# Performance work log

Hardware: AMD Instinct MI355X
Metric: run time of the kernel (lower is better)

The kernel has to match this reference:

```python
import jax, jax.numpy as jnp
import numpy as np

NQ = 18          # num_qubits
DEPTH = 3        # circuit_depth
DIM = 2 ** NQ    # state-vector length
STATE_DIM = 256
HIDDEN = 64
ACTION_DIM = 18
BATCH = 4096


def _apply_1q(sv, g, q):
    # apply 2x2 gate g to qubit q (qubit 0 = most-significant index bit, matching the kron order)
    pre, post = 2 ** q, 2 ** (NQ - q - 1)
    s = sv.reshape(pre, 2, post)
    return jnp.einsum('ab,ibj->iaj', g, s).reshape(-1)


def _apply_cnot(sv, at):
    # CNOT with target at reshape-axis `at`, control at axis `at+1` (adjacent, control less significant)
    pre, post = 2 ** at, 2 ** (NQ - at - 2)
    s = sv.reshape(pre, 2, 2, post)           # (pre, target, control, post)
    out = jnp.stack([s[:, :, 0, :], s[:, ::-1, 1, :]], axis=2)
    return out.reshape(-1)


def _circuit(theta, xc):
    sv = jnp.zeros(DIM, jnp.complex64).at[0].set(1.0)
    th = theta.reshape(DEPTH, NQ, 3)
    for layer in range(DEPTH):
        for q in range(NQ):
            a, b, c = th[layer, q, 0], th[layer, q, 1], th[layer, q, 2]
            ca = jnp.cos(a / 2).astype(jnp.complex64)
            sa = jnp.sin(a / 2).astype(jnp.complex64)
            rx = jnp.stack([jnp.stack([ca, -1j * sa]), jnp.stack([-1j * sa, ca])])
            cb = jnp.cos(b / 2).astype(jnp.complex64)
            sb = jnp.sin(b / 2).astype(jnp.complex64)
            ry = jnp.stack([jnp.stack([cb, -sb]), jnp.stack([sb, cb])])
            ez = jnp.exp(-0.5j * c.astype(jnp.complex64))
            z0 = jnp.zeros_like(ez)
            rz = jnp.stack([jnp.stack([ez, z0]), jnp.stack([z0, jnp.conj(ez)])])
            sv = _apply_1q(sv, rx, q)
            sv = _apply_1q(sv, ry, q)
            sv = _apply_1q(sv, rz, q)
        # original CNOT uses little-endian bit positions: control=q -> axis NQ-1-q, target=q+1 -> axis NQ-2-q
        for q in range(NQ - 1):
            sv = _apply_cnot(sv, NQ - 2 - q)
    # _encode_classical_input: flatten, normalize, add into state prefix, renormalize
    x = xc.reshape(-1)
    xn = jnp.linalg.norm(x)
    x = jnp.where(xn > 0, x / xn.astype(jnp.complex64), x)
    m = min(DIM, x.shape[0])
    sv = sv.at[:m].add(x[:m])
    return sv / jnp.linalg.norm(sv).astype(jnp.complex64)


def setup_inputs() -> dict:
    key = jax.random.key(0)
    ks = jax.random.split(key, 16)
    r = lambda k, shp, s: jax.random.normal(k, shp, jnp.float32) * s
    return {
        'state': r(ks[0], (BATCH, STATE_DIM), 1.0),
        'enc_w1': r(ks[1], (STATE_DIM, HIDDEN), 0.06),
        'enc_b1': jnp.zeros((HIDDEN,), jnp.float32),
        'enc_w2': r(ks[2], (HIDDEN, 2 * NQ), 0.12),
        'enc_b2': jnp.zeros((2 * NQ,), jnp.float32),
        'qparams': r(ks[3], (DEPTH * NQ * 3,), 0.1),
        'dec_w1': r(ks[4], (2 * DIM, HIDDEN), 0.0015),
        'dec_b1': jnp.zeros((HIDDEN,), jnp.float32),
        'dec_w2': r(ks[5], (HIDDEN, ACTION_DIM), 0.12),
        'dec_b2': jnp.zeros((ACTION_DIM,), jnp.float32),
        'val_w1': r(ks[6], (2 * DIM, HIDDEN), 0.0015),
        'val_b1': jnp.zeros((HIDDEN,), jnp.float32),
        'val_w2': r(ks[7], (HIDDEN, 1), 0.12),
        'val_b2': jnp.zeros((1,), jnp.float32),
    }


def reference(state, enc_w1, enc_b1, enc_w2, enc_b2, qparams,
              dec_w1, dec_b1, dec_w2, dec_b2,
              val_w1, val_b1, val_w2, val_b2):
    h = jax.nn.relu(state @ enc_w1 + enc_b1)
    enc = h @ enc_w2 + enc_b2                     # [B, 2*NQ]
    amp, ph = enc[:, :NQ], enc[:, NQ:]
    xc = amp.astype(jnp.complex64) * jnp.exp(1j * ph.astype(jnp.complex64))  # torch.polar
    sv = _circuit(qparams, xc)                    # [2^NQ] complex64
    cl = jnp.concatenate([sv.real, sv.imag])      # [2^(NQ+1)] float32
    logits = jax.nn.relu(cl @ dec_w1 + dec_b1) @ dec_w2 + dec_b2
    value = jax.nn.relu(cl @ val_w1 + val_b1) @ val_w2 + val_b2
    return logits, value
```

## Files before the change

kernel.cpp:

```cpp
#include <hip/hip_runtime.h>
#include <cstdint>
#include <cstddef>


#define NQb   18
#define DIMSZ 262144
#define PMASK 0x3FFFF
#define XLEN  73728

typedef float2 cplx;
typedef float f4 __attribute__((ext_vector_type(4)));

__device__ __forceinline__ cplx cmul(cplx a, cplx b) {
  return make_float2(a.x*b.x - a.y*b.y, a.x*b.y + a.y*b.x);
}
__device__ __forceinline__ cplx cadd(cplx a, cplx b) {
  return make_float2(a.x + b.x, a.y + b.y);
}

__global__ void k_prep(const float* __restrict__ qp, cplx* __restrict__ Ug,
                       cplx* __restrict__ prodLow, cplx* __restrict__ prodHigh,
                       float* __restrict__ accs) {
  __shared__ cplx Ush[54][4];
  int t = threadIdx.x;
  for (int k = t; k < 4352; k += 256) accs[k] = 0.0f;
  if (t < 54) {
    float a = qp[t*3+0], b = qp[t*3+1], c = qp[t*3+2];
    float ca = cosf(0.5f*a), sa = sinf(0.5f*a);
    float cb = cosf(0.5f*b), sb = sinf(0.5f*b);
    float cc = cosf(0.5f*c), sc = sinf(0.5f*c);
    cplx m00 = make_float2( cb*ca,  sb*sa);
    cplx m01 = make_float2(-sb*ca, -cb*sa);
    cplx m10 = make_float2( sb*ca, -cb*sa);
    cplx m11 = make_float2( cb*ca, -sb*sa);
    cplx e0 = make_float2(cc, -sc), e1 = make_float2(cc, sc);
    cplx u00 = cmul(e0, m00), u01 = cmul(e0, m01);
    cplx u10 = cmul(e1, m10), u11 = cmul(e1, m11);
    Ush[t][0] = u00; Ush[t][1] = u01; Ush[t][2] = u10; Ush[t][3] = u11;
    Ug[t*4+0] = u00; Ug[t*4+1] = u01; Ug[t*4+2] = u10; Ug[t*4+3] = u11;
  }
  __syncthreads();
  for (int m = t; m < 4096; m += blockDim.x) {
    cplx v = make_float2(1.f, 0.f);
    for (int p = 0; p < 12; ++p) {
      int q = 17 - p;
      cplx f = ((m >> p) & 1) ? Ush[q][2] : Ush[q][0];
      v = cmul(v, f);
    }
    prodLow[m] = v;
  }
  if (t < 64) {
    cplx v = make_float2(1.f, 0.f);
    for (int p = 12; p < 18; ++p) {
      int q = 17 - p;
      cplx f = ((t >> (p - 12)) & 1) ? Ush[q][2] : Ush[q][0];
      v = cmul(v, f);
    }
    prodHigh[t] = v;
  }
}

__global__ __launch_bounds__(256) void k_enc(
    const float* __restrict__ state, const float* __restrict__ w1,
    const float* __restrict__ b1, const float* __restrict__ w2,
    const float* __restrict__ b2, float* __restrict__ xRe,
    float* __restrict__ xIm, float* __restrict__ xn2) {
  __shared__ float sState[4][256];
  __shared__ float hS[4][64];
  __shared__ float encS[4][36];
  __shared__ float wsum[4];
  int t = threadIdx.x;
  int r = t >> 6, j = t & 63;
  const float4* st4 =
      reinterpret_cast<const float4*>(state + (size_t)blockIdx.x * 1024);
  reinterpret_cast<float4*>(&sState[0][0])[t] = st4[t];
  __syncthreads();
  float a0 = 0.f, a1 = 0.f, a2 = 0.f, a3 = 0.f;
#pragma unroll 4
  for (int k = 0; k < 256; k += 4) {
    a0 = fmaf(sState[r][k+0], w1[(k+0)*64 + j], a0);
    a1 = fmaf(sState[r][k+1], w1[(k+1)*64 + j], a1);
    a2 = fmaf(sState[r][k+2], w1[(k+2)*64 + j], a2);
    a3 = fmaf(sState[r][k+3], w1[(k+3)*64 + j], a3);
  }
  hS[r][j] = fmaxf((a0 + a1) + (a2 + a3) + b1[j], 0.f);
  __syncthreads();
  if (j < 36) {
    float a = b2[j];
#pragma unroll 8
    for (int k = 0; k < 64; ++k) a = fmaf(hS[r][k], w2[k*36 + j], a);
    encS[r][j] = a;
  }
  __syncthreads();
  float lsum = 0.f;
  if (j < 18) {
    float amp = encS[r][j], ph = encS[r][18 + j];
    float sp, cp;
    sincosf(ph, &sp, &cp);
    int row = blockIdx.x*4 + r;
    xRe[row*18 + j] = amp * cp;
    xIm[row*18 + j] = amp * sp;
    lsum = amp * amp;
  }
  for (int off = 32; off > 0; off >>= 1) lsum += __shfl_down(lsum, off, 64);
  if (j == 0) wsum[r] = lsum;
  __syncthreads();
  if (t == 0) atomicAdd(xn2, wsum[0] + wsum[1] + wsum[2] + wsum[3]);
}

__global__ __launch_bounds__(512) void k_gatesLow(
    const cplx* __restrict__ Ug, const cplx* __restrict__ prodLow,
    const cplx* __restrict__ prodHigh, const cplx* __restrict__ svIn,
    cplx* __restrict__ svOut, int layer, int mode) {
  __shared__ float sRe[1024], sIm[1024];
  int t = threadIdx.x;
  int base = blockIdx.x << 10;
  for (int e = t; e < 1024; e += 512) {
    int i = base + e;
    int src = (i ^ (i << 1)) & PMASK;
    cplx v;
    if (mode == 0) v = cmul(prodHigh[src >> 12], prodLow[src & 4095]);
    else           v = svIn[src];
    sRe[e] = v.x; sIm[e] = v.y;
  }
  __syncthreads();
  for (int p = 0; p < 10; ++p) {
    int q = 17 - p;
    const cplx* U = Ug + (layer*18 + q)*4;
    cplx u00 = U[0], u01 = U[1], u10 = U[2], u11 = U[3];
    {
      int k = t;
      int i0 = ((k >> p) << (p + 1)) | (k & ((1 << p) - 1));
      int i1 = i0 | (1 << p);
      cplx a = make_float2(sRe[i0], sIm[i0]);
      cplx b = make_float2(sRe[i1], sIm[i1]);
      cplx na = cadd(cmul(u00, a), cmul(u01, b));
      cplx nb = cadd(cmul(u10, a), cmul(u11, b));
      sRe[i0] = na.x; sIm[i0] = na.y;
      sRe[i1] = nb.x; sIm[i1] = nb.y;
    }
    __syncthreads();
  }
  for (int e = t; e < 1024; e += 512)
    svOut[base + e] = make_float2(sRe[e], sIm[e]);
}

__global__ __launch_bounds__(512) void k_gatesHigh(
    const cplx* __restrict__ Ug, cplx* __restrict__ sv, int layer) {
  __shared__ float tRe[1024], tIm[1024];
  int t = threadIdx.x;
  int l0 = blockIdx.x << 2;
  for (int e = t; e < 1024; e += 512) {
    int h = e >> 2, j = e & 3;
    cplx v = sv[h*1024 + l0 + j];
    tRe[e] = v.x; tIm[e] = v.y;
  }
  __syncthreads();
  for (int ph = 0; ph < 8; ++ph) {
    int q = 7 - ph;
    const cplx* U = Ug + (layer*18 + q)*4;
    cplx u00 = U[0], u01 = U[1], u10 = U[2], u11 = U[3];
    {
      int kh = t >> 2, j = t & 3;
      int h0 = ((kh >> ph) << (ph + 1)) | (kh & ((1 << ph) - 1));
      int h1 = h0 | (1 << ph);
      int i0 = h0*4 + j, i1 = h1*4 + j;
      cplx a = make_float2(tRe[i0], tIm[i0]);
      cplx b = make_float2(tRe[i1], tIm[i1]);
      cplx na = cadd(cmul(u00, a), cmul(u01, b));
      cplx nb = cadd(cmul(u10, a), cmul(u11, b));
      tRe[i0] = na.x; tIm[i0] = na.y;
      tRe[i1] = nb.x; tIm[i1] = nb.y;
    }
    __syncthreads();
  }
  for (int e = t; e < 1024; e += 512) {
    int h = e >> 2, j = e & 3;
    sv[h*1024 + l0 + j] = make_float2(tRe[e], tIm[e]);
  }
}

__global__ __launch_bounds__(256) void k_combine(
    const cplx* __restrict__ svIn, const float* __restrict__ xRe,
    const float* __restrict__ xIm, const float* __restrict__ xn2,
    float* __restrict__ cl, float* __restrict__ L2acc) {
  int t = threadIdx.x;
  float xs = xn2[0];
  float invXn = (xs > 0.f) ? (1.0f / sqrtf(xs)) : 1.0f;
  float lsum = 0.f;
  for (int u = 0; u < 4; ++u) {
    int i = blockIdx.x*1024 + u*256 + t;
    int src = (i ^ (i << 1)) & PMASK;
    cplx v = svIn[src];
    if (i < XLEN) {
      v.x = fmaf(xRe[i], invXn, v.x);
      v.y = fmaf(xIm[i], invXn, v.y);
    }
    cl[i] = v.x;
    cl[DIMSZ + i] = v.y;
    lsum += v.x*v.x + v.y*v.y;
  }
  for (int off = 32; off > 0; off >>= 1) lsum += __shfl_down(lsum, off, 64);
  if ((t & 63) == 0) atomicAdd(L2acc, lsum);
}

#define GLOAD(dst, ptr) \
  asm volatile("global_load_dwordx4 %0, %1, off nt" : "=v"(dst) : "v"(ptr))

#define VMWAIT(N, x0,x1,x2,x3,x4,x5,x6,x7) do {                      \
    asm volatile("s_waitcnt vmcnt(" #N ")"                           \
        : "+v"(x0), "+v"(x1), "+v"(x2), "+v"(x3),                    \
          "+v"(x4), "+v"(x5), "+v"(x6), "+v"(x7));                   \
    __builtin_amdgcn_sched_barrier(0);                               \
  } while (0)

#define CONSUME(g, w0,w1,w2,w3,w4,w5,w6,w7) do {                     \
    const int rr = (g)*128 + ro;                                     \
    float s0 = clS[rr+  0], s1 = clS[rr+ 16];                        \
    float s2 = clS[rr+ 32], s3 = clS[rr+ 48];                        \
    float s4 = clS[rr+ 64], s5 = clS[rr+ 80];                        \
    float s6 = clS[rr+ 96], s7 = clS[rr+112];                        \
    ax = fmaf(s0, w0[0], ax); ay = fmaf(s0, w0[1], ay);              \
    az = fmaf(s0, w0[2], az); aw = fmaf(s0, w0[3], aw);              \
    ax = fmaf(s1, w1[0], ax); ay = fmaf(s1, w1[1], ay);              \
    az = fmaf(s1, w1[2], az); aw = fmaf(s1, w1[3], aw);              \
    ax = fmaf(s2, w2[0], ax); ay = fmaf(s2, w2[1], ay);              \
    az = fmaf(s2, w2[2], az); aw = fmaf(s2, w2[3], aw);              \
    ax = fmaf(s3, w3[0], ax); ay = fmaf(s3, w3[1], ay);              \
    az = fmaf(s3, w3[2], az); aw = fmaf(s3, w3[3], aw);              \
    ax = fmaf(s4, w4[0], ax); ay = fmaf(s4, w4[1], ay);              \
    az = fmaf(s4, w4[2], az); aw = fmaf(s4, w4[3], aw);              \
    ax = fmaf(s5, w5[0], ax); ay = fmaf(s5, w5[1], ay);              \
    az = fmaf(s5, w5[2], az); aw = fmaf(s5, w5[3], aw);              \
    ax = fmaf(s6, w6[0], ax); ay = fmaf(s6, w6[1], ay);              \
    az = fmaf(s6, w6[2], az); aw = fmaf(s6, w6[3], aw);              \
    ax = fmaf(s7, w7[0], ax); ay = fmaf(s7, w7[1], ay);              \
    az = fmaf(s7, w7[2], az); aw = fmaf(s7, w7[3], aw);              \
  } while (0)

__global__ __launch_bounds__(256) void k_matvec(
    const float* __restrict__ cl, const float* __restrict__ Wdec,
    const float* __restrict__ Wval, float* __restrict__ dots_rep) {
  __shared__ float clS[512];
  __shared__ float red[1024];
  int t = threadIdx.x;
  int mat = blockIdx.x & 1;
  int chunk = blockIdx.x >> 1;
  size_t r0 = (size_t)chunk * 512;
  if (t < 128)
    reinterpret_cast<float4*>(clS)[t] =
        reinterpret_cast<const float4*>(cl + r0)[t];
  __syncthreads();
  const float* Wb = (mat ? Wval : Wdec) + r0*64 + (size_t)((t & 15)*4);
  const int ro = t >> 4;
  const float* p0 = Wb + (size_t)ro * 64;
  const float* p1 = p0 + 1024;
  const float* p2 = p0 + 2048;
  const float* p3 = p0 + 3072;
  const float* p4 = p0 + 4096;
  const float* p5 = p0 + 5120;
  const float* p6 = p0 + 6144;
  const float* p7 = p0 + 7168;
  float ax = 0.f, ay = 0.f, az = 0.f, aw = 0.f;
  f4 A0, A1, A2, A3, A4, A5, A6, A7;
  f4 B0, B1, B2, B3, B4, B5, B6, B7;
  GLOAD(A0, p0);        GLOAD(A1, p1);        GLOAD(A2, p2);
  GLOAD(A3, p3);        GLOAD(A4, p4);        GLOAD(A5, p5);
  GLOAD(A6, p6);        GLOAD(A7, p7);
  GLOAD(B0, p0 + 8192); GLOAD(B1, p1 + 8192); GLOAD(B2, p2 + 8192);
  GLOAD(B3, p3 + 8192); GLOAD(B4, p4 + 8192); GLOAD(B5, p5 + 8192);
  GLOAD(B6, p6 + 8192); GLOAD(B7, p7 + 8192);
  VMWAIT(8, A0, A1, A2, A3, A4, A5, A6, A7);
  CONSUME(0, A0, A1, A2, A3, A4, A5, A6, A7);
  GLOAD(A0, p0 + 16384); GLOAD(A1, p1 + 16384); GLOAD(A2, p2 + 16384);
  GLOAD(A3, p3 + 16384); GLOAD(A4, p4 + 16384); GLOAD(A5, p5 + 16384);
  GLOAD(A6, p6 + 16384); GLOAD(A7, p7 + 16384);
  VMWAIT(8, B0, B1, B2, B3, B4, B5, B6, B7);
  CONSUME(1, B0, B1, B2, B3, B4, B5, B6, B7);
  GLOAD(B0, p0 + 24576); GLOAD(B1, p1 + 24576); GLOAD(B2, p2 + 24576);
  GLOAD(B3, p3 + 24576); GLOAD(B4, p4 + 24576); GLOAD(B5, p5 + 24576);
  GLOAD(B6, p6 + 24576); GLOAD(B7, p7 + 24576);
  VMWAIT(8, A0, A1, A2, A3, A4, A5, A6, A7);
  CONSUME(2, A0, A1, A2, A3, A4, A5, A6, A7);
  VMWAIT(0, B0, B1, B2, B3, B4, B5, B6, B7);
  CONSUME(3, B0, B1, B2, B3, B4, B5, B6, B7);

  red[t*4+0] = ax; red[t*4+1] = ay; red[t*4+2] = az; red[t*4+3] = aw;
  __syncthreads();
  if (t < 64) {
    int ci0 = t >> 2, jj = t & 3;
    float sum = 0.f;
#pragma unroll
    for (int r2 = 0; r2 < 16; ++r2) sum += red[(r2*16 + ci0)*4 + jj];
    int slot = chunk & 31;
    atomicAdd(&dots_rep[slot*128 + mat*64 + t], sum);
  }
}

__global__ void k_final(const float* __restrict__ dots_rep,
                        const float* __restrict__ L2acc,
                        const float* __restrict__ db1,
                        const float* __restrict__ dw2,
                        const float* __restrict__ db2,
                        const float* __restrict__ vb1,
                        const float* __restrict__ vw2,
                        const float* __restrict__ vb2,
                        float* __restrict__ out) {
  __shared__ float hd[64], hv[64];
  int t = threadIdx.x;
  float sd = 0.f, sva = 0.f;
#pragma unroll
  for (int s = 0; s < 32; ++s) {
    sd  += dots_rep[s*128 + t];
    sva += dots_rep[s*128 + 64 + t];
  }
  float invL = 1.0f / sqrtf(L2acc[0]);
  hd[t] = fmaxf(sd * invL + db1[t], 0.f);
  hv[t] = fmaxf(sva * invL + vb1[t], 0.f);
  __syncthreads();
  if (t < 18) {
    float s = db2[t];
    for (int k = 0; k < 64; ++k) s = fmaf(hd[k], dw2[k*18 + t], s);
    out[t] = s;
  }
  if (t == 20) {
    float s = vb2[0];
    for (int k = 0; k < 64; ++k) s = fmaf(hv[k], vw2[k], s);
    out[18] = s;
  }
}

extern "C" void kernel_launch(void* const* d_in, const int* in_sizes, int n_in,
                              void* d_out, int out_size, void* d_ws,
                              size_t ws_size, hipStream_t stream) {
  const float* state  = (const float*)d_in[0];
  const float* enc_w1 = (const float*)d_in[1];
  const float* enc_b1 = (const float*)d_in[2];
  const float* enc_w2 = (const float*)d_in[3];
  const float* enc_b2 = (const float*)d_in[4];
  const float* qparams= (const float*)d_in[5];
  const float* dec_w1 = (const float*)d_in[6];
  const float* dec_b1 = (const float*)d_in[7];
  const float* dec_w2 = (const float*)d_in[8];
  const float* dec_b2 = (const float*)d_in[9];
  const float* val_w1 = (const float*)d_in[10];
  const float* val_b1 = (const float*)d_in[11];
  const float* val_w2 = (const float*)d_in[12];
  const float* val_b2 = (const float*)d_in[13];

  float* wsf = (float*)d_ws;
  float* dots_rep = wsf;
  float* xn2      = wsf + 4096;
  float* L2acc    = wsf + 4097;
  cplx*  Ug       = (cplx*)(wsf + 4352);
  cplx*  prodLow  = (cplx*)(wsf + 8192);
  cplx*  prodHigh = (cplx*)(wsf + 16384);
  float* xRe      = wsf + 16640;
  float* xIm      = wsf + 90368;
  cplx*  svA      = (cplx*)(wsf + 164096);
  cplx*  svB      = (cplx*)(wsf + 688384);
  float* cl       = wsf + 1212672;

  hipLaunchKernelGGL(k_prep, dim3(1), dim3(256), 0, stream,
                     qparams, Ug, prodLow, prodHigh, wsf);
  hipLaunchKernelGGL(k_enc, dim3(1024), dim3(256), 0, stream,
                     state, enc_w1, enc_b1, enc_w2, enc_b2, xRe, xIm, xn2);
  hipLaunchKernelGGL(k_gatesLow, dim3(256), dim3(512), 0, stream,
                     Ug, prodLow, prodHigh, (const cplx*)nullptr, svA, 1, 0);
  hipLaunchKernelGGL(k_gatesHigh, dim3(256), dim3(512), 0, stream, Ug, svA, 1);
  hipLaunchKernelGGL(k_gatesLow, dim3(256), dim3(512), 0, stream,
                     Ug, prodLow, prodHigh, (const cplx*)svA, svB, 2, 1);
  hipLaunchKernelGGL(k_gatesHigh, dim3(256), dim3(512), 0, stream, Ug, svB, 2);
  hipLaunchKernelGGL(k_combine, dim3(256), dim3(256), 0, stream,
                     svB, xRe, xIm, xn2, cl, L2acc);
  hipLaunchKernelGGL(k_matvec, dim3(2048), dim3(256), 0, stream,
                     cl, dec_w1, val_w1, dots_rep);
  hipLaunchKernelGGL(k_final, dim3(1), dim3(64), 0, stream,
                     dots_rep, L2acc, dec_b1, dec_w2, dec_b2,
                     val_b1, val_w2, val_b2, (float*)d_out);
}
```

Baseline: 355.3 us.

## Fuse state-vector combine into matvec and parallelize prep across blocks

The separate combine kernel, which un-permuted the state vector, added the encoded input and wrote a real/imag `cl` buffer, is removed. Each matvec block now builds its 512-element slice of `cl` in shared memory directly from the state vector and accumulates the L2 norm. The prep kernel's 4096-entry product table is spread over 16 blocks instead of one. This drops one launch and a 2 MB write/read round trip, but each state-vector element is now read twice (once per dec/val matrix) with a strided gather.

```diff
diff --git a/kernel.cpp b/kernel.cpp
--- a/kernel.cpp
+++ b/kernel.cpp
@@ -23,7 +23,9 @@
                        float* __restrict__ accs) {
   __shared__ cplx Ush[54][4];
   int t = threadIdx.x;
-  for (int k = t; k < 4352; k += 256) accs[k] = 0.0f;
+  int blk = blockIdx.x;
+  if (blk == 0)
+    for (int k = t; k < 4352; k += 256) accs[k] = 0.0f;
   if (t < 54) {
     float a = qp[t*3+0], b = qp[t*3+1], c = qp[t*3+2];
     float ca = cosf(0.5f*a), sa = sinf(0.5f*a);
@@ -37,10 +39,13 @@
     cplx u00 = cmul(e0, m00), u01 = cmul(e0, m01);
     cplx u10 = cmul(e1, m10), u11 = cmul(e1, m11);
     Ush[t][0] = u00; Ush[t][1] = u01; Ush[t][2] = u10; Ush[t][3] = u11;
-    Ug[t*4+0] = u00; Ug[t*4+1] = u01; Ug[t*4+2] = u10; Ug[t*4+3] = u11;
-  }
-  __syncthreads();
-  for (int m = t; m < 4096; m += blockDim.x) {
+    if (blk == 0) {
+      Ug[t*4+0] = u00; Ug[t*4+1] = u01; Ug[t*4+2] = u10; Ug[t*4+3] = u11;
+    }
+  }
+  __syncthreads();
+  {
+    int m = blk*256 + t;
     cplx v = make_float2(1.f, 0.f);
     for (int p = 0; p < 12; ++p) {
       int q = 17 - p;
@@ -49,7 +54,7 @@
     }
     prodLow[m] = v;
   }
-  if (t < 64) {
+  if (blk == 0 && t < 64) {
     cplx v = make_float2(1.f, 0.f);
     for (int p = 12; p < 18; ++p) {
       int q = 17 - p;
@@ -178,30 +183,6 @@
     int h = e >> 2, j = e & 3;
     sv[h*1024 + l0 + j] = make_float2(tRe[e], tIm[e]);
   }
-}
-
-__global__ __launch_bounds__(256) void k_combine(
-    const cplx* __restrict__ svIn, const float* __restrict__ xRe,
-    const float* __restrict__ xIm, const float* __restrict__ xn2,
-    float* __restrict__ cl, float* __restrict__ L2acc) {
-  int t = threadIdx.x;
-  float xs = xn2[0];
-  float invXn = (xs > 0.f) ? (1.0f / sqrtf(xs)) : 1.0f;
-  float lsum = 0.f;
-  for (int u = 0; u < 4; ++u) {
-    int i = blockIdx.x*1024 + u*256 + t;
-    int src = (i ^ (i << 1)) & PMASK;
-    cplx v = svIn[src];
-    if (i < XLEN) {
-      v.x = fmaf(xRe[i], invXn, v.x);
-      v.y = fmaf(xIm[i], invXn, v.y);
-    }
-    cl[i] = v.x;
-    cl[DIMSZ + i] = v.y;
-    lsum += v.x*v.x + v.y*v.y;
-  }
-  for (int off = 32; off > 0; off >>= 1) lsum += __shfl_down(lsum, off, 64);
-  if ((t & 63) == 0) atomicAdd(L2acc, lsum);
 }
 
 #define GLOAD(dst, ptr) \
@@ -239,18 +220,44 @@
   } while (0)
 
 __global__ __launch_bounds__(256) void k_matvec(
-    const float* __restrict__ cl, const float* __restrict__ Wdec,
-    const float* __restrict__ Wval, float* __restrict__ dots_rep) {
+    const cplx* __restrict__ svIn, const float* __restrict__ xRe,
+    const float* __restrict__ xIm, const float* __restrict__ xn2,
+    const float* __restrict__ Wdec, const float* __restrict__ Wval,
+    float* __restrict__ dots_rep, float* __restrict__ L2acc) {
   __shared__ float clS[512];
   __shared__ float red[1024];
+  __shared__ float blkL2[4];
   int t = threadIdx.x;
   int mat = blockIdx.x & 1;
   int chunk = blockIdx.x >> 1;
+  int plane = chunk >> 9;
+  int idx0 = (chunk & 511) << 9;
+  {
+    int i0 = idx0 + t*2;
+    int s0 = ( i0      ^ ( i0      << 1)) & PMASK;
+    int s1 = ((i0 + 1) ^ ((i0 + 1) << 1)) & PMASK;
+    cplx a = svIn[s0], b = svIn[s1];
+    float v0 = plane ? a.y : a.x;
+    float v1 = plane ? b.y : b.x;
+    if (idx0 < XLEN) {
+      float xs = xn2[0];
+      float invXn = (xs > 0.f) ? (1.0f / sqrtf(xs)) : 1.0f;
+      const float* xsrc = plane ? xIm : xRe;
+      v0 = fmaf(xsrc[i0],     invXn, v0);
+      v1 = fmaf(xsrc[i0 + 1], invXn, v1);
+    }
+    clS[t*2]     = v0;
+    clS[t*2 + 1] = v1;
+    if (mat == 0) {
+      float ls = v0*v0 + v1*v1;
+      for (int off = 32; off > 0; off >>= 1) ls += __shfl_down(ls, off, 64);
+      if ((t & 63) == 0) blkL2[t >> 6] = ls;
+    }
+  }
+  __syncthreads();
+  if (mat == 0 && t == 0)
+    atomicAdd(L2acc, blkL2[0] + blkL2[1] + blkL2[2] + blkL2[3]);
   size_t r0 = (size_t)chunk * 512;
-  if (t < 128)
-    reinterpret_cast<float4*>(clS)[t] =
-        reinterpret_cast<const float4*>(cl + r0)[t];
-  __syncthreads();
   const float* Wb = (mat ? Wval : Wdec) + r0*64 + (size_t)((t & 15)*4);
   const int ro = t >> 4;
   const float* p0 = Wb + (size_t)ro * 64;
@@ -359,9 +366,8 @@
   float* xIm      = wsf + 90368;
   cplx*  svA      = (cplx*)(wsf + 164096);
   cplx*  svB      = (cplx*)(wsf + 688384);
-  float* cl       = wsf + 1212672;
-
-  hipLaunchKernelGGL(k_prep, dim3(1), dim3(256), 0, stream,
+
+  hipLaunchKernelGGL(k_prep, dim3(16), dim3(256), 0, stream,
                      qparams, Ug, prodLow, prodHigh, wsf);
   hipLaunchKernelGGL(k_enc, dim3(1024), dim3(256), 0, stream,
                      state, enc_w1, enc_b1, enc_w2, enc_b2, xRe, xIm, xn2);
@@ -371,10 +377,8 @@
   hipLaunchKernelGGL(k_gatesLow, dim3(256), dim3(512), 0, stream,
                      Ug, prodLow, prodHigh, (const cplx*)svA, svB, 2, 1);
   hipLaunchKernelGGL(k_gatesHigh, dim3(256), dim3(512), 0, stream, Ug, svB, 2);
-  hipLaunchKernelGGL(k_combine, dim3(256), dim3(256), 0, stream,
-                     svB, xRe, xIm, xn2, cl, L2acc);
   hipLaunchKernelGGL(k_matvec, dim3(2048), dim3(256), 0, stream,
-                     cl, dec_w1, val_w1, dots_rep);
+                     svB, xRe, xIm, xn2, dec_w1, val_w1, dots_rep, L2acc);
   hipLaunchKernelGGL(k_final, dim3(1), dim3(64), 0, stream,
                      dots_rep, L2acc, dec_b1, dec_w2, dec_b2,
                      val_b1, val_w2, val_b2, (float*)d_out);
```

Measured after the change: 344.7 us. 1.03x faster.
